# Performance work log

Measured on AMD Instinct MI355X. Metric: run time of the kernel, lower is better.

Reference implementation:

```python
import jax, jax.numpy as jnp
import numpy as np

B, NP, NS, CIN, COUT, CMID = 16, 1024, 32, 64, 128, 32

def _bn(x, g, b, m, v, eps=1e-5):
    # inference-mode BatchNorm over channel axis 1
    sh = (1, -1) + (1,) * (x.ndim - 2)
    return (x - m.reshape(sh)) * (g.reshape(sh) * jax.lax.rsqrt(v.reshape(sh) + eps)) + b.reshape(sh)

def setup_inputs() -> dict:
    key = jax.random.key(0)
    ks = jax.random.split(key, 10)
    f = jax.random.normal
    return {
        "new_xyz": f(ks[0], (B, 3, NP), jnp.float32),
        "grouped_xyz": f(ks[1], (B, NP, NS, 3), jnp.float32),
        "grouped_feature": f(ks[2], (B, CIN, NS, NP), jnp.float32),
        "wh_w": f(ks[3], (CMID, 3), jnp.float32) * 0.1,
        "wh_b": f(ks[4], (CMID,), jnp.float32) * 0.1,
        "wh_g": jnp.ones((CMID,), jnp.float32), "wh_beta": jnp.zeros((CMID,), jnp.float32),
        "wh_m": jnp.zeros((CMID,), jnp.float32), "wh_v": jnp.ones((CMID,), jnp.float32),
        "n1_w": f(ks[5], (16, 1), jnp.float32) * 0.1,
        "n1_b": f(ks[6], (16,), jnp.float32) * 0.1,
        "n1_g": jnp.ones((16,), jnp.float32), "n1_beta": jnp.zeros((16,), jnp.float32),
        "n1_m": jnp.zeros((16,), jnp.float32), "n1_v": jnp.ones((16,), jnp.float32),
        "n2_w": f(ks[7], (1, 16), jnp.float32) * 0.1,
        "n2_b": f(ks[8], (1,), jnp.float32) * 0.1,
        "n2_g": jnp.ones((1,), jnp.float32), "n2_beta": jnp.zeros((1,), jnp.float32),
        "n2_m": jnp.zeros((1,), jnp.float32), "n2_v": jnp.ones((1,), jnp.float32),
        "out_w": f(ks[9], (COUT, CIN, CMID), jnp.float32) * 0.05,
        "out_b": jnp.zeros((COUT,), jnp.float32),
        "out_g": jnp.ones((COUT,), jnp.float32), "out_beta": jnp.zeros((COUT,), jnp.float32),
        "out_m": jnp.zeros((COUT,), jnp.float32), "out_v": jnp.ones((COUT,), jnp.float32),
    }

def reference(new_xyz, grouped_xyz, grouped_feature,
              wh_w, wh_b, wh_g, wh_beta, wh_m, wh_v,
              n1_w, n1_b, n1_g, n1_beta, n1_m, n1_v,
              n2_w, n2_b, n2_g, n2_beta, n2_m, n2_v,
              out_w, out_b, out_g, out_beta, out_m, out_v):
    # kernel_density_estimation_ball mutates in place: after i=0 the reference
    # point is zero, so ONLY sample 0 is actually zeroed. Replicate exactly.
    gx = grouped_xyz.at[:, :, 0, :].set(0.0)          # [B,NP,NS,3]
    density = jnp.sum(gx, axis=-1, keepdims=True)      # [B,NP,NS,1]
    density = jnp.where(density < 1e-10, 1e-10, density)
    inv = 1.0 / density
    ds = inv / jnp.max(inv, axis=2, keepdims=True)     # [B,NP,NS,1]
    # weight net on the mutated grouped_xyz
    gx_p = jnp.transpose(gx, (0, 3, 1, 2))             # [B,3,NP,NS]
    w = jax.nn.relu(_bn(jnp.einsum('bcps,oc->bops', gx_p, wh_w) + wh_b.reshape(1, -1, 1, 1),
                        wh_g, wh_beta, wh_m, wh_v))    # [B,CMID,NP,NS]
    # nonlinear density transform
    dsp = jnp.transpose(ds, (0, 3, 1, 2))              # [B,1,NP,NS]
    d1 = jax.nn.relu(_bn(jnp.einsum('bcps,oc->bops', dsp, n1_w) + n1_b.reshape(1, -1, 1, 1),
                         n1_g, n1_beta, n1_m, n1_v))   # [B,16,NP,NS]
    d2 = jax.nn.sigmoid(_bn(jnp.einsum('bcps,oc->bops', d1, n2_w) + n2_b.reshape(1, -1, 1, 1),
                            n2_g, n2_beta, n2_m, n2_v))  # [B,1,NP,NS]
    # density-scaled features, then batched matmul with positional weights
    gf = jnp.transpose(grouped_feature, (0, 1, 3, 2)) * d2      # [B,CIN,NP,NS]
    mm = jnp.einsum('bcps,bmps->bcpm', gf, w)                   # [B,CIN,NP,CMID]
    # out_conv: Conv2d(CIN->COUT, kernel (1,CMID)) collapses last dim
    out = jnp.einsum('bcpk,ock->bop', mm, out_w) + out_b.reshape(1, -1, 1)  # [B,COUT,NP]
    out = _bn(out, out_g, out_beta, out_m, out_v)
    return (jnp.transpose(new_xyz, (0, 2, 1)), out)
```

## Files before the change

### kernel.cpp

```cpp
#include <hip/hip_runtime.h>
#include <hip/hip_bf16.h>


#define NPP 1024

typedef __attribute__((ext_vector_type(8))) short short8;
typedef __attribute__((ext_vector_type(4))) float f32x4;

__device__ __forceinline__ unsigned short f2bf(float x) {
  union { float f; unsigned u; } v; v.f = x;
  unsigned r = v.u + 0x7FFFu + ((v.u >> 16) & 1u);
  return (unsigned short)(r >> 16);
}

__device__ __forceinline__ unsigned long long pack4bf(f32x4 v) {
  return (unsigned long long)f2bf(v[0])
       | ((unsigned long long)f2bf(v[1]) << 16)
       | ((unsigned long long)f2bf(v[2]) << 32)
       | ((unsigned long long)f2bf(v[3]) << 48);
}

__global__ __launch_bounds__(256) void k_prep(
    const float* __restrict__ out_w, const float* __restrict__ new_xyz,
    unsigned short* __restrict__ owc, float* __restrict__ out0)
{
  int bid = blockIdx.x, t = threadIdx.x;
  if (bid < 128) {
    int gid = bid * 256 + t;
    int lane = gid & 63, ci = gid >> 6;
    int hi = ci & 1, tt = (ci >> 1) & 15, cblk = (ci >> 5) & 3, w = ci >> 7;
    int sg = lane >> 4, l15 = lane & 15;
    int o = w*32 + hi*16 + l15;
    int k = tt*2 + (sg >> 1);
    int cbase = cblk*16 + (sg & 1)*8;
    short8 vv;
    #pragma unroll
    for (int j = 0; j < 8; ++j)
      vv[j] = (short)f2bf(out_w[(o*64 + cbase + j)*32 + k]);
    *(short8*)&owc[(size_t)gid * 8] = vv;
  } else {
    int idx = (bid - 128) * 256 + t;
    int b = idx / 3072, r = idx - b*3072, p = r / 3, d = r - p*3;
    out0[idx] = new_xyz[(b*3 + d)*NPP + p];
  }
}

struct Smem3 {
  union {
    struct {
      float gxd[64*32*4];
      unsigned short wd[16*32*32];
    } ph0;
    unsigned short fs[32768];
  } u;
  char mm[64*1024];
  float cst[192];
};

__global__ __launch_bounds__(512, 1) void k_main(
    const float* __restrict__ F, const float* __restrict__ GX,
    const float* __restrict__ whw, const float* __restrict__ whb,
    const float* __restrict__ whg, const float* __restrict__ whbeta,
    const float* __restrict__ whm, const float* __restrict__ whv,
    const float* __restrict__ n1w, const float* __restrict__ n1b,
    const float* __restrict__ n1g, const float* __restrict__ n1beta,
    const float* __restrict__ n1m, const float* __restrict__ n1v,
    const float* __restrict__ n2w, const float* __restrict__ n2b,
    const float* __restrict__ n2g, const float* __restrict__ n2beta,
    const float* __restrict__ n2m, const float* __restrict__ n2v,
    const unsigned short* __restrict__ OWc,
    const float* __restrict__ ob, const float* __restrict__ og,
    const float* __restrict__ obeta, const float* __restrict__ om,
    const float* __restrict__ ov,
    float* __restrict__ out1)
{
  __shared__ Smem3 sm;
  int xcd = blockIdx.x & 7, idx = blockIdx.x >> 3;
  int b = xcd*2 + (idx >> 4), pt64 = idx & 15;
  int p0 = pt64 * 64;
  int t = threadIdx.x, w = t >> 6, lane = t & 63;
  int l15 = lane & 15, sg = lane >> 4;

  int so = w & 3, ch = w >> 2;
  int q4 = lane & 3, c3 = (lane >> 2) & 7, jh = (lane >> 5) & 1;
  int c_l = ch*8 + c3, s0 = so*8 + jh*4;
  const float* fsrc0 = &F[((size_t)((b*64 + c_l)*32) + s0)*NPP + p0 + q4*4];

  float4 fv[4][4];
  #pragma unroll
  for (int jj = 0; jj < 4; ++jj)
    #pragma unroll
    for (int qg = 0; qg < 4; ++qg)
      fv[jj][qg] = *(const float4*)&fsrc0[(size_t)jj*NPP + qg*16];

  int pp8 = t >> 3, si8 = t & 7;
  const float* g = &GX[(size_t)(b*NPP + p0 + pp8)*96 + si8*12];
  float4 f0 = *(const float4*)g;
  float4 f1 = *(const float4*)(g + 4);
  float4 f2 = *(const float4*)(g + 8);

  if (t < 32) {
    float sc = whg[t] * rsqrtf(whv[t] + 1e-5f);
    sm.cst[t]    = whw[t*3+0] * sc;
    sm.cst[32+t] = whw[t*3+1] * sc;
    sm.cst[64+t] = whw[t*3+2] * sc;
    sm.cst[96+t] = (whb[t] - whm[t]) * sc + whbeta[t];
  } else if (t < 48) {
    int i = t - 32;
    float sc = n1g[i] * rsqrtf(n1v[i] + 1e-5f);
    sm.cst[128+i] = n1w[i] * sc;
    sm.cst[144+i] = (n1b[i] - n1m[i]) * sc + n1beta[i];
  } else if (t < 64) {
    int i = t - 48;
    float sc = n2g[0] * rsqrtf(n2v[0] + 1e-5f);
    sm.cst[160+i] = n2w[i] * sc;
    if (i == 0) sm.cst[176] = (n2b[0] - n2m[0]) * sc + n2beta[0];
  }
  __syncthreads();

  {
    float xs[4], ys[4], zs[4], inv[4];
    xs[0]=f0.x; ys[0]=f0.y; zs[0]=f0.z;
    xs[1]=f0.w; ys[1]=f1.x; zs[1]=f1.y;
    xs[2]=f1.z; ys[2]=f1.w; zs[2]=f2.x;
    xs[3]=f2.y; ys[3]=f2.z; zs[3]=f2.w;
    if (si8 == 0) { xs[0]=0.f; ys[0]=0.f; zs[0]=0.f; }
    float mx = 0.f;
    #pragma unroll
    for (int u = 0; u < 4; ++u) {
      float den = xs[u] + ys[u] + zs[u];
      if (den < 1e-10f) den = 1e-10f;
      inv[u] = 1.0f / den;
      mx = fmaxf(mx, inv[u]);
    }
    #pragma unroll
    for (int m = 1; m < 8; m <<= 1) mx = fmaxf(mx, __shfl_xor(mx, m, 8));
    #pragma unroll
    for (int u = 0; u < 4; ++u) {
      float ds = inv[u] / mx;
      float acc = sm.cst[176];
      #pragma unroll
      for (int i = 0; i < 16; ++i) {
        float d1 = fmaxf(ds * sm.cst[128+i] + sm.cst[144+i], 0.f);
        acc += d1 * sm.cst[160+i];
      }
      float d2 = 1.0f / (1.0f + expf(-acc));
      float4 st = {xs[u], ys[u], zs[u], d2};
      *(float4*)&sm.u.ph0.gxd[(size_t)(pp8*32 + si8*4 + u)*4] = st;
    }
  }
  __syncthreads();

  const f32x4 z4 = {0,0,0,0};
  int phKh = (lane >> 4) & 1;
  int phPp = w*2 + (lane >> 5);
  int phSi = lane & 15;
  int ppA = w*2, ppB = w*2 + 1;
  int c0 = l15*32 + sg*8;

  short8 bfrA[4][2], bfrB[4][2];
  #pragma unroll
  for (int pg = 0; pg < 4; ++pg) {
    const float4 ga = *(const float4*)&sm.u.ph0.gxd[(size_t)((pg*16 + phPp)*32 + phSi*2)*4];
    const float4 gb = *(const float4*)&sm.u.ph0.gxd[(size_t)((pg*16 + phPp)*32 + phSi*2 + 1)*4];
    #pragma unroll
    for (int ki = 0; ki < 16; ++ki) {
      int k = phKh*16 + ki;
      float a0 = sm.cst[k], a1 = sm.cst[32+k], a2 = sm.cst[64+k], bc = sm.cst[96+k];
      float w0 = fmaxf(ga.x*a0 + ga.y*a1 + ga.z*a2 + bc, 0.f) * ga.w;
      float w1 = fmaxf(gb.x*a0 + gb.y*a1 + gb.z*a2 + bc, 0.f) * gb.w;
      unsigned r = (unsigned)f2bf(w0) | ((unsigned)f2bf(w1) << 16);
      *(unsigned*)&sm.u.ph0.wd[(phPp*32 + k)*32 + phSi*2] = r;
    }
    #pragma unroll
    for (int kh = 0; kh < 2; ++kh) {
      bfrA[pg][kh] = *(const short8*)&sm.u.ph0.wd[(ppA*32 + kh*16 + l15)*32 + sg*8];
      bfrB[pg][kh] = *(const short8*)&sm.u.ph0.wd[(ppB*32 + kh*16 + l15)*32 + sg*8];
    }
  }
  __syncthreads();

  int w4 = w & 3, gp0 = (w >> 2) * 2;
  f32x4 acc00 = {0,0,0,0}, acc10 = {0,0,0,0}, acc01 = {0,0,0,0}, acc11 = {0,0,0,0};
  int rowG0 = gp0*16 + l15, rowG1 = (gp0+1)*16 + l15;
  unsigned sw0 = (rowG0 & 15) << 4, sw1 = (rowG1 & 15) << 4;
  const char* bbase0 = sm.mm + rowG0*1024;
  const char* bbase1 = sm.mm + rowG1*1024;
  int fsbase = so*128 + c_l*8 + jh*4;

  #pragma unroll
  for (int cblk = 0; cblk < 4; ++cblk) {
    #pragma unroll
    for (int qg = 0; qg < 4; ++qg)
      #pragma unroll
      for (int pi = 0; pi < 4; ++pi) {
        int p = qg*16 + q4*4 + pi;
        unsigned sw = (unsigned)(p & 15) << 3;
        #pragma unroll
        for (int jp = 0; jp < 2; ++jp) {
          unsigned u = (unsigned)f2bf(((const float*)&fv[jp*2][qg])[pi])
                     | ((unsigned)f2bf(((const float*)&fv[jp*2+1][qg])[pi]) << 16);
          unsigned fidx = (unsigned)(p*512 + fsbase + jp*2) ^ sw;
          *(unsigned*)&sm.u.fs[fidx] = u;
        }
      }
    __syncthreads();

    short8 afA[4], afB[4];
    unsigned swA = (unsigned)(ppA & 15) << 3, swB = (unsigned)(ppB & 15) << 3;
    #pragma unroll
    for (int pg = 0; pg < 4; ++pg) {
      unsigned iA = (unsigned)((pg*16 + ppA)*512 + sg*128 + l15*8) ^ swA;
      unsigned iB = (unsigned)((pg*16 + ppB)*512 + sg*128 + l15*8) ^ swB;
      afA[pg] = *(const short8*)&sm.u.fs[iA];
      afB[pg] = *(const short8*)&sm.u.fs[iB];
    }
    if (cblk < 3) {
      const float* fsrc = fsrc0 + (size_t)(cblk + 1) * 16 * 32 * NPP;
      #pragma unroll
      for (int jj = 0; jj < 4; ++jj)
        #pragma unroll
        for (int qg = 0; qg < 4; ++qg)
          fv[jj][qg] = *(const float4*)&fsrc[(size_t)jj*NPP + qg*16];
    }
    #pragma unroll
    for (int pg = 0; pg < 4; ++pg) {
      f32x4 mA0 = __builtin_amdgcn_mfma_f32_16x16x32_bf16(afA[pg], bfrA[pg][0], z4, 0,0,0);
      f32x4 mA1 = __builtin_amdgcn_mfma_f32_16x16x32_bf16(afA[pg], bfrA[pg][1], z4, 0,0,0);
      f32x4 mB0 = __builtin_amdgcn_mfma_f32_16x16x32_bf16(afB[pg], bfrB[pg][0], z4, 0,0,0);
      f32x4 mB1 = __builtin_amdgcn_mfma_f32_16x16x32_bf16(afB[pg], bfrB[pg][1], z4, 0,0,0);
      int rowA = pg*16 + ppA, rowB = pg*16 + ppB;
      unsigned swa = (rowA & 15) << 4, swb = (rowB & 15) << 4;
      char* bA = sm.mm + rowA*1024;
      char* bB = sm.mm + rowB*1024;
      *(unsigned long long*)(bA + ((c0      ) ^ swa)) = pack4bf(mA0);
      *(unsigned long long*)(bA + ((c0 + 512) ^ swa)) = pack4bf(mA1);
      *(unsigned long long*)(bB + ((c0      ) ^ swb)) = pack4bf(mB0);
      *(unsigned long long*)(bB + ((c0 + 512) ^ swb)) = pack4bf(mB1);
    }
    __syncthreads();
    {
      const unsigned short* ac = &OWc[(size_t)((w4*4 + cblk)*16)*1024 + lane*8];
      #pragma unroll 8
      for (int tt = 0; tt < 16; ++tt) {
        short8 a0 = *(const short8*)&ac[tt*1024];
        short8 a1 = *(const short8*)&ac[tt*1024 + 512];
        int col = sg*16 + tt*64;
        short8 b0 = *(const short8*)(bbase0 + (col ^ sw0));
        short8 b1 = *(const short8*)(bbase1 + (col ^ sw1));
        acc00 = __builtin_amdgcn_mfma_f32_16x16x32_bf16(a0, b0, acc00, 0,0,0);
        acc10 = __builtin_amdgcn_mfma_f32_16x16x32_bf16(a1, b0, acc10, 0,0,0);
        acc01 = __builtin_amdgcn_mfma_f32_16x16x32_bf16(a0, b1, acc01, 0,0,0);
        acc11 = __builtin_amdgcn_mfma_f32_16x16x32_bf16(a1, b1, acc11, 0,0,0);
      }
    }
    __syncthreads();
  }

  #pragma unroll
  for (int hi = 0; hi < 2; ++hi)
    #pragma unroll
    for (int gg = 0; gg < 2; ++gg) {
      f32x4 a = hi ? (gg ? acc11 : acc10) : (gg ? acc01 : acc00);
      #pragma unroll
      for (int r = 0; r < 4; ++r) {
        int o = w4*32 + hi*16 + sg*4 + r;
        float sc = og[o] * rsqrtf(ov[o] + 1e-5f);
        float dd = (ob[o] - om[o]) * sc + obeta[o];
        out1[(size_t)(b*128 + o)*NPP + p0 + (gp0+gg)*16 + l15] = a[r] * sc + dd;
      }
    }
}

extern "C" void kernel_launch(void* const* d_in, const int* in_sizes, int n_in,
                              void* d_out, int out_size, void* d_ws, size_t ws_size,
                              hipStream_t stream) {
  (void)in_sizes; (void)n_in; (void)out_size; (void)ws_size;
  const float* new_xyz = (const float*)d_in[0];
  const float* gxyz    = (const float*)d_in[1];
  const float* gfeat   = (const float*)d_in[2];
  const float* whw     = (const float*)d_in[3];
  const float* whb     = (const float*)d_in[4];
  const float* whg     = (const float*)d_in[5];
  const float* whbeta  = (const float*)d_in[6];
  const float* whm     = (const float*)d_in[7];
  const float* whv     = (const float*)d_in[8];
  const float* n1w     = (const float*)d_in[9];
  const float* n1b     = (const float*)d_in[10];
  const float* n1g     = (const float*)d_in[11];
  const float* n1beta  = (const float*)d_in[12];
  const float* n1m     = (const float*)d_in[13];
  const float* n1v     = (const float*)d_in[14];
  const float* n2w     = (const float*)d_in[15];
  const float* n2b     = (const float*)d_in[16];
  const float* n2g     = (const float*)d_in[17];
  const float* n2beta  = (const float*)d_in[18];
  const float* n2m     = (const float*)d_in[19];
  const float* n2v     = (const float*)d_in[20];
  const float* out_w   = (const float*)d_in[21];
  const float* out_b   = (const float*)d_in[22];
  const float* out_g   = (const float*)d_in[23];
  const float* out_bt  = (const float*)d_in[24];
  const float* out_m   = (const float*)d_in[25];
  const float* out_v   = (const float*)d_in[26];

  unsigned short* owc = (unsigned short*)d_ws;
  float* out0 = (float*)d_out;
  float* out1 = out0 + 16*1024*3;

  hipLaunchKernelGGL(k_prep, dim3(320), dim3(256), 0, stream, out_w, new_xyz, owc, out0);
  hipLaunchKernelGGL(k_main, dim3(256), dim3(512), 0, stream,
      gfeat, gxyz, whw, whb, whg, whbeta, whm, whv,
      n1w, n1b, n1g, n1beta, n1m, n1v,
      n2w, n2b, n2g, n2beta, n2m, n2v,
      owc, out_b, out_g, out_bt, out_m, out_v, out1);
}
```

Baseline: 70.97 us.

## Halve per-block point tile to 32 and shrink LDS for multi-block occupancy

Each block now handles 32 points instead of 64, which doubles the grid to 512 blocks. The LDS layout is reorganised into two unions: one overlaps the gxd and fs buffers, the other overlaps wd and mm. This cuts shared memory per block roughly in half, and launch bounds now ask for 4 blocks per CU. The aim is to fill all CUs with more resident waves and hide the latency of the global feature loads. The cost is that each out_w fragment loaded from global is reused over half as many points, so weight traffic per point doubles, and only half the threads do the density prep.

```diff
diff --git a/kernel.cpp b/kernel.cpp
--- a/kernel.cpp
+++ b/kernel.cpp
@@ -45,19 +45,19 @@
   }
 }
 
-struct Smem3 {
+struct Smem4 {
   union {
-    struct {
-      float gxd[64*32*4];
-      unsigned short wd[16*32*32];
-    } ph0;
-    unsigned short fs[32768];
-  } u;
-  char mm[64*1024];
+    float gxd[32*32*4];
+    unsigned short fs[16384];
+  } a;
+  union {
+    unsigned short wd[16*32*32];
+    char mm[32*1024];
+  } bu;
   float cst[192];
 };
 
-__global__ __launch_bounds__(512, 1) void k_main(
+__global__ __launch_bounds__(512, 4) void k_main(
     const float* __restrict__ F, const float* __restrict__ GX,
     const float* __restrict__ whw, const float* __restrict__ whb,
     const float* __restrict__ whg, const float* __restrict__ whbeta,
@@ -74,10 +74,10 @@
     const float* __restrict__ ov,
     float* __restrict__ out1)
 {
-  __shared__ Smem3 sm;
+  __shared__ Smem4 sm;
   int xcd = blockIdx.x & 7, idx = blockIdx.x >> 3;
-  int b = xcd*2 + (idx >> 4), pt64 = idx & 15;
-  int p0 = pt64 * 64;
+  int b = xcd*2 + (idx >> 5), pt32 = idx & 31;
+  int p0 = pt32 * 32;
   int t = threadIdx.x, w = t >> 6, lane = t & 63;
   int l15 = lane & 15, sg = lane >> 4;
 
@@ -86,18 +86,12 @@
   int c_l = ch*8 + c3, s0 = so*8 + jh*4;
   const float* fsrc0 = &F[((size_t)((b*64 + c_l)*32) + s0)*NPP + p0 + q4*4];
 
-  float4 fv[4][4];
+  float4 fv[4][2];
   #pragma unroll
   for (int jj = 0; jj < 4; ++jj)
     #pragma unroll
-    for (int qg = 0; qg < 4; ++qg)
+    for (int qg = 0; qg < 2; ++qg)
       fv[jj][qg] = *(const float4*)&fsrc0[(size_t)jj*NPP + qg*16];
-
-  int pp8 = t >> 3, si8 = t & 7;
-  const float* g = &GX[(size_t)(b*NPP + p0 + pp8)*96 + si8*12];
-  float4 f0 = *(const float4*)g;
-  float4 f1 = *(const float4*)(g + 4);
-  float4 f2 = *(const float4*)(g + 8);
 
   if (t < 32) {
     float sc = whg[t] * rsqrtf(whv[t] + 1e-5f);
@@ -118,7 +112,12 @@
   }
   __syncthreads();
 
-  {
+  if (t < 256) {
+    int pp8 = t >> 3, si8 = t & 7;
+    const float* g = &GX[(size_t)(b*NPP + p0 + pp8)*96 + si8*12];
+    float4 f0 = *(const float4*)g;
+    float4 f1 = *(const float4*)(g + 4);
+    float4 f2 = *(const float4*)(g + 8);
     float xs[4], ys[4], zs[4], inv[4];
     xs[0]=f0.x; ys[0]=f0.y; zs[0]=f0.z;
     xs[1]=f0.w; ys[1]=f1.x; zs[1]=f1.y;
@@ -146,7 +145,7 @@
       }
       float d2 = 1.0f / (1.0f + expf(-acc));
       float4 st = {xs[u], ys[u], zs[u], d2};
-      *(float4*)&sm.u.ph0.gxd[(size_t)(pp8*32 + si8*4 + u)*4] = st;
+      *(float4*)&sm.a.gxd[(size_t)(pp8*32 + si8*4 + u)*4] = st;
     }
   }
   __syncthreads();
@@ -158,11 +157,11 @@
   int ppA = w*2, ppB = w*2 + 1;
   int c0 = l15*32 + sg*8;
 
-  short8 bfrA[4][2], bfrB[4][2];
+  short8 bfrA[2][2], bfrB[2][2];
   #pragma unroll
-  for (int pg = 0; pg < 4; ++pg) {
-    const float4 ga = *(const float4*)&sm.u.ph0.gxd[(size_t)((pg*16 + phPp)*32 + phSi*2)*4];
-    const float4 gb = *(const float4*)&sm.u.ph0.gxd[(size_t)((pg*16 + phPp)*32 + phSi*2 + 1)*4];
+  for (int pg = 0; pg < 2; ++pg) {
+    const float4 ga = *(const float4*)&sm.a.gxd[(size_t)((pg*16 + phPp)*32 + phSi*2)*4];
+    const float4 gb = *(const float4*)&sm.a.gxd[(size_t)((pg*16 + phPp)*32 + phSi*2 + 1)*4];
     #pragma unroll
     for (int ki = 0; ki < 16; ++ki) {
       int k = phKh*16 + ki;
@@ -170,28 +169,27 @@
       float w0 = fmaxf(ga.x*a0 + ga.y*a1 + ga.z*a2 + bc, 0.f) * ga.w;
       float w1 = fmaxf(gb.x*a0 + gb.y*a1 + gb.z*a2 + bc, 0.f) * gb.w;
       unsigned r = (unsigned)f2bf(w0) | ((unsigned)f2bf(w1) << 16);
-      *(unsigned*)&sm.u.ph0.wd[(phPp*32 + k)*32 + phSi*2] = r;
+      *(unsigned*)&sm.bu.wd[(phPp*32 + k)*32 + phSi*2] = r;
     }
     #pragma unroll
     for (int kh = 0; kh < 2; ++kh) {
-      bfrA[pg][kh] = *(const short8*)&sm.u.ph0.wd[(ppA*32 + kh*16 + l15)*32 + sg*8];
-      bfrB[pg][kh] = *(const short8*)&sm.u.ph0.wd[(ppB*32 + kh*16 + l15)*32 + sg*8];
+      bfrA[pg][kh] = *(const short8*)&sm.bu.wd[(ppA*32 + kh*16 + l15)*32 + sg*8];
+      bfrB[pg][kh] = *(const short8*)&sm.bu.wd[(ppB*32 + kh*16 + l15)*32 + sg*8];
     }
   }
   __syncthreads();
 
-  int w4 = w & 3, gp0 = (w >> 2) * 2;
-  f32x4 acc00 = {0,0,0,0}, acc10 = {0,0,0,0}, acc01 = {0,0,0,0}, acc11 = {0,0,0,0};
-  int rowG0 = gp0*16 + l15, rowG1 = (gp0+1)*16 + l15;
-  unsigned sw0 = (rowG0 & 15) << 4, sw1 = (rowG1 & 15) << 4;
-  const char* bbase0 = sm.mm + rowG0*1024;
-  const char* bbase1 = sm.mm + rowG1*1024;
+  int w4 = w & 3, gp = w >> 2;
+  f32x4 acc0 = {0,0,0,0}, acc1 = {0,0,0,0};
+  int rowG = gp*16 + l15;
+  unsigned swG = (unsigned)(rowG & 15) << 4;
+  const char* bbase = sm.bu.mm + rowG*1024;
   int fsbase = so*128 + c_l*8 + jh*4;
 
   #pragma unroll
   for (int cblk = 0; cblk < 4; ++cblk) {
     #pragma unroll
-    for (int qg = 0; qg < 4; ++qg)
+    for (int qg = 0; qg < 2; ++qg)
       #pragma unroll
       for (int pi = 0; pi < 4; ++pi) {
         int p = qg*16 + q4*4 + pi;
@@ -201,38 +199,38 @@
           unsigned u = (unsigned)f2bf(((const float*)&fv[jp*2][qg])[pi])
                      | ((unsigned)f2bf(((const float*)&fv[jp*2+1][qg])[pi]) << 16);
           unsigned fidx = (unsigned)(p*512 + fsbase + jp*2) ^ sw;
-          *(unsigned*)&sm.u.fs[fidx] = u;
+          *(unsigned*)&sm.a.fs[fidx] = u;
         }
       }
     __syncthreads();
 
-    short8 afA[4], afB[4];
+    short8 afA[2], afB[2];
     unsigned swA = (unsigned)(ppA & 15) << 3, swB = (unsigned)(ppB & 15) << 3;
     #pragma unroll
-    for (int pg = 0; pg < 4; ++pg) {
+    for (int pg = 0; pg < 2; ++pg) {
       unsigned iA = (unsigned)((pg*16 + ppA)*512 + sg*128 + l15*8) ^ swA;
       unsigned iB = (unsigned)((pg*16 + ppB)*512 + sg*128 + l15*8) ^ swB;
-      afA[pg] = *(const short8*)&sm.u.fs[iA];
-      afB[pg] = *(const short8*)&sm.u.fs[iB];
+      afA[pg] = *(const short8*)&sm.a.fs[iA];
+      afB[pg] = *(const short8*)&sm.a.fs[iB];
     }
     if (cblk < 3) {
       const float* fsrc = fsrc0 + (size_t)(cblk + 1) * 16 * 32 * NPP;
       #pragma unroll
       for (int jj = 0; jj < 4; ++jj)
         #pragma unroll
-        for (int qg = 0; qg < 4; ++qg)
+        for (int qg = 0; qg < 2; ++qg)
           fv[jj][qg] = *(const float4*)&fsrc[(size_t)jj*NPP + qg*16];
     }
     #pragma unroll
-    for (int pg = 0; pg < 4; ++pg) {
+    for (int pg = 0; pg < 2; ++pg) {
       f32x4 mA0 = __builtin_amdgcn_mfma_f32_16x16x32_bf16(afA[pg], bfrA[pg][0], z4, 0,0,0);
       f32x4 mA1 = __builtin_amdgcn_mfma_f32_16x16x32_bf16(afA[pg], bfrA[pg][1], z4, 0,0,0);
       f32x4 mB0 = __builtin_amdgcn_mfma_f32_16x16x32_bf16(afB[pg], bfrB[pg][0], z4, 0,0,0);
       f32x4 mB1 = __builtin_amdgcn_mfma_f32_16x16x32_bf16(afB[pg], bfrB[pg][1], z4, 0,0,0);
       int rowA = pg*16 + ppA, rowB = pg*16 + ppB;
-      unsigned swa = (rowA & 15) << 4, swb = (rowB & 15) << 4;
-      char* bA = sm.mm + rowA*1024;
-      char* bB = sm.mm + rowB*1024;
+      unsigned swa = (unsigned)(rowA & 15) << 4, swb = (unsigned)(rowB & 15) << 4;
+      char* bA = sm.bu.mm + rowA*1024;
+      char* bB = sm.bu.mm + rowB*1024;
       *(unsigned long long*)(bA + ((c0      ) ^ swa)) = pack4bf(mA0);
       *(unsigned long long*)(bA + ((c0 + 512) ^ swa)) = pack4bf(mA1);
       *(unsigned long long*)(bB + ((c0      ) ^ swb)) = pack4bf(mB0);
@@ -246,30 +244,25 @@
         short8 a0 = *(const short8*)&ac[tt*1024];
         short8 a1 = *(const short8*)&ac[tt*1024 + 512];
         int col = sg*16 + tt*64;
-        short8 b0 = *(const short8*)(bbase0 + (col ^ sw0));
-        short8 b1 = *(const short8*)(bbase1 + (col ^ sw1));
-        acc00 = __builtin_amdgcn_mfma_f32_16x16x32_bf16(a0, b0, acc00, 0,0,0);
-        acc10 = __builtin_amdgcn_mfma_f32_16x16x32_bf16(a1, b0, acc10, 0,0,0);
-        acc01 = __builtin_amdgcn_mfma_f32_16x16x32_bf16(a0, b1, acc01, 0,0,0);
-        acc11 = __builtin_amdgcn_mfma_f32_16x16x32_bf16(a1, b1, acc11, 0,0,0);
+        short8 bb = *(const short8*)(bbase + (col ^ swG));
+        acc0 = __builtin_amdgcn_mfma_f32_16x16x32_bf16(a0, bb, acc0, 0,0,0);
+        acc1 = __builtin_amdgcn_mfma_f32_16x16x32_bf16(a1, bb, acc1, 0,0,0);
       }
     }
     __syncthreads();
   }
 
   #pragma unroll
-  for (int hi = 0; hi < 2; ++hi)
-    #pragma unroll
-    for (int gg = 0; gg < 2; ++gg) {
-      f32x4 a = hi ? (gg ? acc11 : acc10) : (gg ? acc01 : acc00);
-      #pragma unroll
-      for (int r = 0; r < 4; ++r) {
-        int o = w4*32 + hi*16 + sg*4 + r;
-        float sc = og[o] * rsqrtf(ov[o] + 1e-5f);
-        float dd = (ob[o] - om[o]) * sc + obeta[o];
-        out1[(size_t)(b*128 + o)*NPP + p0 + (gp0+gg)*16 + l15] = a[r] * sc + dd;
-      }
-    }
+  for (int hi = 0; hi < 2; ++hi) {
+    f32x4 a = hi ? acc1 : acc0;
+    #pragma unroll
+    for (int r = 0; r < 4; ++r) {
+      int o = w4*32 + hi*16 + sg*4 + r;
+      float sc = og[o] * rsqrtf(ov[o] + 1e-5f);
+      float dd = (ob[o] - om[o]) * sc + obeta[o];
+      out1[(size_t)(b*128 + o)*NPP + p0 + gp*16 + l15] = a[r] * sc + dd;
+    }
+  }
 }
 
 extern "C" void kernel_launch(void* const* d_in, const int* in_sizes, int n_in,
@@ -309,7 +302,7 @@
   float* out1 = out0 + 16*1024*3;
 
   hipLaunchKernelGGL(k_prep, dim3(320), dim3(256), 0, stream, out_w, new_xyz, owc, out0);
-  hipLaunchKernelGGL(k_main, dim3(256), dim3(512), 0, stream,
+  hipLaunchKernelGGL(k_main, dim3(512), dim3(512), 0, stream,
       gfeat, gxyz, whw, whb, whg, whbeta, whm, whv,
       n1w, n1b, n1g, n1beta, n1m, n1v,
       n2w, n2b, n2g, n2beta, n2m, n2v,
```

Result: slower. 76.16 us (+7.3%).

## Split fused kernel into two stages with global bf16 intermediate

Applied to the files above, without the earlier changes.

The single fused kernel is split. The first stage computes the density-weighted feature-by-positional-weight matmul and writes the bf16 result to a global workspace. A second kernel with 1024 blocks of 256 threads then loads it into LDS and runs the output-conv MFMA plus BatchNorm. This is meant to remove the serialized second GEMM and the extra barriers inside each 256-block kernel, and to give stage 2 more parallelism. In exchange it adds a global write and read of the intermediate (about 64MB of bf16) and one more kernel launch.

```diff
diff --git a/kernel.cpp b/kernel.cpp
--- a/kernel.cpp
+++ b/kernel.cpp
@@ -45,7 +45,7 @@
   }
 }
 
-struct Smem3 {
+struct SmemS1 {
   union {
     struct {
       float gxd[64*32*4];
@@ -53,11 +53,10 @@
     } ph0;
     unsigned short fs[32768];
   } u;
-  char mm[64*1024];
   float cst[192];
 };
 
-__global__ __launch_bounds__(512, 1) void k_main(
+__global__ __launch_bounds__(512, 1) void k_stage1(
     const float* __restrict__ F, const float* __restrict__ GX,
     const float* __restrict__ whw, const float* __restrict__ whb,
     const float* __restrict__ whg, const float* __restrict__ whbeta,
@@ -68,13 +67,9 @@
     const float* __restrict__ n2w, const float* __restrict__ n2b,
     const float* __restrict__ n2g, const float* __restrict__ n2beta,
     const float* __restrict__ n2m, const float* __restrict__ n2v,
-    const unsigned short* __restrict__ OWc,
-    const float* __restrict__ ob, const float* __restrict__ og,
-    const float* __restrict__ obeta, const float* __restrict__ om,
-    const float* __restrict__ ov,
-    float* __restrict__ out1)
+    unsigned short* __restrict__ mmG)
 {
-  __shared__ Smem3 sm;
+  __shared__ SmemS1 sm;
   int xcd = blockIdx.x & 7, idx = blockIdx.x >> 3;
   int b = xcd*2 + (idx >> 4), pt64 = idx & 15;
   int p0 = pt64 * 64;
@@ -156,7 +151,6 @@
   int phPp = w*2 + (lane >> 5);
   int phSi = lane & 15;
   int ppA = w*2, ppB = w*2 + 1;
-  int c0 = l15*32 + sg*8;
 
   short8 bfrA[4][2], bfrB[4][2];
   #pragma unroll
@@ -180,12 +174,6 @@
   }
   __syncthreads();
 
-  int w4 = w & 3, gp0 = (w >> 2) * 2;
-  f32x4 acc00 = {0,0,0,0}, acc10 = {0,0,0,0}, acc01 = {0,0,0,0}, acc11 = {0,0,0,0};
-  int rowG0 = gp0*16 + l15, rowG1 = (gp0+1)*16 + l15;
-  unsigned sw0 = (rowG0 & 15) << 4, sw1 = (rowG1 & 15) << 4;
-  const char* bbase0 = sm.mm + rowG0*1024;
-  const char* bbase1 = sm.mm + rowG1*1024;
   int fsbase = so*128 + c_l*8 + jh*4;
 
   #pragma unroll
@@ -229,47 +217,74 @@
       f32x4 mA1 = __builtin_amdgcn_mfma_f32_16x16x32_bf16(afA[pg], bfrA[pg][1], z4, 0,0,0);
       f32x4 mB0 = __builtin_amdgcn_mfma_f32_16x16x32_bf16(afB[pg], bfrB[pg][0], z4, 0,0,0);
       f32x4 mB1 = __builtin_amdgcn_mfma_f32_16x16x32_bf16(afB[pg], bfrB[pg][1], z4, 0,0,0);
-      int rowA = pg*16 + ppA, rowB = pg*16 + ppB;
-      unsigned swa = (rowA & 15) << 4, swb = (rowB & 15) << 4;
-      char* bA = sm.mm + rowA*1024;
-      char* bB = sm.mm + rowB*1024;
-      *(unsigned long long*)(bA + ((c0      ) ^ swa)) = pack4bf(mA0);
-      *(unsigned long long*)(bA + ((c0 + 512) ^ swa)) = pack4bf(mA1);
-      *(unsigned long long*)(bB + ((c0      ) ^ swb)) = pack4bf(mB0);
-      *(unsigned long long*)(bB + ((c0 + 512) ^ swb)) = pack4bf(mB1);
+      int pA = p0 + pg*16 + ppA, pB = p0 + pg*16 + ppB;
+      unsigned short* gA = &mmG[(size_t)(b*1024 + pA)*2048 + cblk*512 + l15*16 + sg*4];
+      unsigned short* gB = &mmG[(size_t)(b*1024 + pB)*2048 + cblk*512 + l15*16 + sg*4];
+      *(unsigned long long*)(gA)       = pack4bf(mA0);
+      *(unsigned long long*)(gA + 256) = pack4bf(mA1);
+      *(unsigned long long*)(gB)       = pack4bf(mB0);
+      *(unsigned long long*)(gB + 256) = pack4bf(mB1);
     }
     __syncthreads();
-    {
-      const unsigned short* ac = &OWc[(size_t)((w4*4 + cblk)*16)*1024 + lane*8];
-      #pragma unroll 8
-      for (int tt = 0; tt < 16; ++tt) {
-        short8 a0 = *(const short8*)&ac[tt*1024];
-        short8 a1 = *(const short8*)&ac[tt*1024 + 512];
-        int col = sg*16 + tt*64;
-        short8 b0 = *(const short8*)(bbase0 + (col ^ sw0));
-        short8 b1 = *(const short8*)(bbase1 + (col ^ sw1));
-        acc00 = __builtin_amdgcn_mfma_f32_16x16x32_bf16(a0, b0, acc00, 0,0,0);
-        acc10 = __builtin_amdgcn_mfma_f32_16x16x32_bf16(a1, b0, acc10, 0,0,0);
-        acc01 = __builtin_amdgcn_mfma_f32_16x16x32_bf16(a0, b1, acc01, 0,0,0);
-        acc11 = __builtin_amdgcn_mfma_f32_16x16x32_bf16(a1, b1, acc11, 0,0,0);
-      }
-    }
-    __syncthreads();
-  }
-
-  #pragma unroll
-  for (int hi = 0; hi < 2; ++hi)
-    #pragma unroll
-    for (int gg = 0; gg < 2; ++gg) {
-      f32x4 a = hi ? (gg ? acc11 : acc10) : (gg ? acc01 : acc00);
-      #pragma unroll
-      for (int r = 0; r < 4; ++r) {
-        int o = w4*32 + hi*16 + sg*4 + r;
-        float sc = og[o] * rsqrtf(ov[o] + 1e-5f);
-        float dd = (ob[o] - om[o]) * sc + obeta[o];
-        out1[(size_t)(b*128 + o)*NPP + p0 + (gp0+gg)*16 + l15] = a[r] * sc + dd;
-      }
-    }
+  }
+}
+
+__global__ __launch_bounds__(256, 2) void k_stage2(
+    const unsigned short* __restrict__ OWc,
+    const unsigned short* __restrict__ mmG,
+    const float* __restrict__ ob, const float* __restrict__ og,
+    const float* __restrict__ obeta, const float* __restrict__ om,
+    const float* __restrict__ ov,
+    float* __restrict__ out1)
+{
+  __shared__ unsigned short ms[16*2048];
+  int xcd = blockIdx.x & 7, idx = blockIdx.x >> 3;
+  int b = xcd*2 + (idx >> 6), ptile = idx & 63;
+  int p0 = ptile * 16;
+  int t = threadIdx.x, w = t >> 6, lane = t & 63;
+  int l15 = lane & 15, sg = lane >> 4;
+
+  #pragma unroll
+  for (int i = 0; i < 4; ++i) {
+    int pl = i*4 + w;
+    const unsigned short* src = &mmG[(size_t)(b*1024 + p0 + pl)*2048 + lane*8];
+    #pragma unroll
+    for (int j = 0; j < 4; ++j) {
+      short8 v = *(const short8*)&src[j*512];
+      unsigned off = ((unsigned)(pl*4096 + lane*16 + j*1024)) ^ ((unsigned)(pl & 15) << 4);
+      *(short8*)((char*)ms + off) = v;
+    }
+  }
+  __syncthreads();
+
+  f32x4 acc0 = {0,0,0,0}, acc1 = {0,0,0,0};
+  unsigned swR = (unsigned)(l15 & 15) << 4;
+  const char* brow = (const char*)ms + l15*4096;
+  #pragma unroll
+  for (int cblk = 0; cblk < 4; ++cblk) {
+    const unsigned short* ac = &OWc[(size_t)((w*4 + cblk)*16)*1024 + lane*8];
+    #pragma unroll 8
+    for (int tt = 0; tt < 16; ++tt) {
+      short8 a0 = *(const short8*)&ac[tt*1024];
+      short8 a1 = *(const short8*)&ac[tt*1024 + 512];
+      unsigned col = (unsigned)(cblk*1024 + tt*64 + sg*16) ^ swR;
+      short8 bb = *(const short8*)(brow + col);
+      acc0 = __builtin_amdgcn_mfma_f32_16x16x32_bf16(a0, bb, acc0, 0,0,0);
+      acc1 = __builtin_amdgcn_mfma_f32_16x16x32_bf16(a1, bb, acc1, 0,0,0);
+    }
+  }
+
+  #pragma unroll
+  for (int hi = 0; hi < 2; ++hi) {
+    f32x4 a = hi ? acc1 : acc0;
+    #pragma unroll
+    for (int r = 0; r < 4; ++r) {
+      int o = w*32 + hi*16 + sg*4 + r;
+      float sc = og[o] * rsqrtf(ov[o] + 1e-5f);
+      float dd = (ob[o] - om[o]) * sc + obeta[o];
+      out1[(size_t)(b*128 + o)*NPP + p0 + l15] = a[r] * sc + dd;
+    }
+  }
 }
 
 extern "C" void kernel_launch(void* const* d_in, const int* in_sizes, int n_in,
@@ -305,13 +320,15 @@
   const float* out_v   = (const float*)d_in[26];
 
   unsigned short* owc = (unsigned short*)d_ws;
+  unsigned short* mmG = owc + (1u << 18);
   float* out0 = (float*)d_out;
   float* out1 = out0 + 16*1024*3;
 
-  hipLaunchKernelGGL(k_prep, dim3(320), dim3(256), 0, stream, out_w, new_xyz, owc, out0);
-  hipLaunchKernelGGL(k_main, dim3(256), dim3(512), 0, stream,
+  hipLaunchKernelGGL(k_prep,   dim3(320),  dim3(256), 0, stream, out_w, new_xyz, owc, out0);
+  hipLaunchKernelGGL(k_stage1, dim3(256),  dim3(512), 0, stream,
       gfeat, gxyz, whw, whb, whg, whbeta, whm, whv,
       n1w, n1b, n1g, n1beta, n1m, n1v,
-      n2w, n2b, n2g, n2beta, n2m, n2v,
-      owc, out_b, out_g, out_bt, out_m, out_v, out1);
-}
+      n2w, n2b, n2g, n2beta, n2m, n2v, mmG);
+  hipLaunchKernelGGL(k_stage2, dim3(1024), dim3(256), 0, stream,
+      owc, mmG, out_b, out_g, out_bt, out_m, out_v, out1);
+}
```

Result: slower. 94.77 us (+33.5%).

## Alias mm buffer onto feature staging LDS and drop register prefetch to raise occupancy

Applied to the files above, without the earlier changes.

Removes the separate 64KB mm shared buffer by reusing the feature staging buffer, which needs an extra barrier between reading the A fragments and writing mm. The 64-float4 register prefetch of the next channel block is dropped; features are loaded in two halves right before conversion. Launch bounds change to allow more blocks per CU. This trades the overlap of global loads with compute for lower LDS and register use, so several blocks can hide latency instead.

```diff
diff --git a/kernel.cpp b/kernel.cpp
--- a/kernel.cpp
+++ b/kernel.cpp
@@ -45,19 +45,18 @@
   }
 }
 
-struct Smem3 {
+struct Smem6 {
   union {
     struct {
       float gxd[64*32*4];
       unsigned short wd[16*32*32];
     } ph0;
-    unsigned short fs[32768];
+    unsigned short fsmm[32768];
   } u;
-  char mm[64*1024];
   float cst[192];
 };
 
-__global__ __launch_bounds__(512, 1) void k_main(
+__global__ __launch_bounds__(512, 4) void k_main(
     const float* __restrict__ F, const float* __restrict__ GX,
     const float* __restrict__ whw, const float* __restrict__ whb,
     const float* __restrict__ whg, const float* __restrict__ whbeta,
@@ -74,7 +73,7 @@
     const float* __restrict__ ov,
     float* __restrict__ out1)
 {
-  __shared__ Smem3 sm;
+  __shared__ Smem6 sm;
   int xcd = blockIdx.x & 7, idx = blockIdx.x >> 3;
   int b = xcd*2 + (idx >> 4), pt64 = idx & 15;
   int p0 = pt64 * 64;
@@ -85,13 +84,6 @@
   int q4 = lane & 3, c3 = (lane >> 2) & 7, jh = (lane >> 5) & 1;
   int c_l = ch*8 + c3, s0 = so*8 + jh*4;
   const float* fsrc0 = &F[((size_t)((b*64 + c_l)*32) + s0)*NPP + p0 + q4*4];
-
-  float4 fv[4][4];
-  #pragma unroll
-  for (int jj = 0; jj < 4; ++jj)
-    #pragma unroll
-    for (int qg = 0; qg < 4; ++qg)
-      fv[jj][qg] = *(const float4*)&fsrc0[(size_t)jj*NPP + qg*16];
 
   int pp8 = t >> 3, si8 = t & 7;
   const float* g = &GX[(size_t)(b*NPP + p0 + pp8)*96 + si8*12];
@@ -184,26 +176,36 @@
   f32x4 acc00 = {0,0,0,0}, acc10 = {0,0,0,0}, acc01 = {0,0,0,0}, acc11 = {0,0,0,0};
   int rowG0 = gp0*16 + l15, rowG1 = (gp0+1)*16 + l15;
   unsigned sw0 = (rowG0 & 15) << 4, sw1 = (rowG1 & 15) << 4;
-  const char* bbase0 = sm.mm + rowG0*1024;
-  const char* bbase1 = sm.mm + rowG1*1024;
+  const char* bbase0 = (const char*)sm.u.fsmm + rowG0*1024;
+  const char* bbase1 = (const char*)sm.u.fsmm + rowG1*1024;
   int fsbase = so*128 + c_l*8 + jh*4;
 
   #pragma unroll
   for (int cblk = 0; cblk < 4; ++cblk) {
     #pragma unroll
-    for (int qg = 0; qg < 4; ++qg)
+    for (int half = 0; half < 2; ++half) {
+      float4 fvh[4][2];
+      const float* fsrc = fsrc0 + (size_t)cblk * 16 * 32 * NPP;
       #pragma unroll
-      for (int pi = 0; pi < 4; ++pi) {
-        int p = qg*16 + q4*4 + pi;
-        unsigned sw = (unsigned)(p & 15) << 3;
+      for (int jj = 0; jj < 4; ++jj)
         #pragma unroll
-        for (int jp = 0; jp < 2; ++jp) {
-          unsigned u = (unsigned)f2bf(((const float*)&fv[jp*2][qg])[pi])
-                     | ((unsigned)f2bf(((const float*)&fv[jp*2+1][qg])[pi]) << 16);
-          unsigned fidx = (unsigned)(p*512 + fsbase + jp*2) ^ sw;
-          *(unsigned*)&sm.u.fs[fidx] = u;
+        for (int qh = 0; qh < 2; ++qh)
+          fvh[jj][qh] = *(const float4*)&fsrc[(size_t)jj*NPP + (half*2 + qh)*16];
+      #pragma unroll
+      for (int qh = 0; qh < 2; ++qh)
+        #pragma unroll
+        for (int pi = 0; pi < 4; ++pi) {
+          int p = (half*2 + qh)*16 + q4*4 + pi;
+          unsigned sw = (unsigned)(p & 15) << 3;
+          #pragma unroll
+          for (int jp = 0; jp < 2; ++jp) {
+            unsigned u = (unsigned)f2bf(((const float*)&fvh[jp*2][qh])[pi])
+                       | ((unsigned)f2bf(((const float*)&fvh[jp*2+1][qh])[pi]) << 16);
+            unsigned fidx = (unsigned)(p*512 + fsbase + jp*2) ^ sw;
+            *(unsigned*)&sm.u.fsmm[fidx] = u;
+          }
         }
-      }
+    }
     __syncthreads();
 
     short8 afA[4], afB[4];
@@ -212,17 +214,11 @@
     for (int pg = 0; pg < 4; ++pg) {
       unsigned iA = (unsigned)((pg*16 + ppA)*512 + sg*128 + l15*8) ^ swA;
       unsigned iB = (unsigned)((pg*16 + ppB)*512 + sg*128 + l15*8) ^ swB;
-      afA[pg] = *(const short8*)&sm.u.fs[iA];
-      afB[pg] = *(const short8*)&sm.u.fs[iB];
-    }
-    if (cblk < 3) {
-      const float* fsrc = fsrc0 + (size_t)(cblk + 1) * 16 * 32 * NPP;
-      #pragma unroll
-      for (int jj = 0; jj < 4; ++jj)
-        #pragma unroll
-        for (int qg = 0; qg < 4; ++qg)
-          fv[jj][qg] = *(const float4*)&fsrc[(size_t)jj*NPP + qg*16];
-    }
+      afA[pg] = *(const short8*)&sm.u.fsmm[iA];
+      afB[pg] = *(const short8*)&sm.u.fsmm[iB];
+    }
+    __syncthreads();
+
     #pragma unroll
     for (int pg = 0; pg < 4; ++pg) {
       f32x4 mA0 = __builtin_amdgcn_mfma_f32_16x16x32_bf16(afA[pg], bfrA[pg][0], z4, 0,0,0);
@@ -231,14 +227,15 @@
       f32x4 mB1 = __builtin_amdgcn_mfma_f32_16x16x32_bf16(afB[pg], bfrB[pg][1], z4, 0,0,0);
       int rowA = pg*16 + ppA, rowB = pg*16 + ppB;
       unsigned swa = (rowA & 15) << 4, swb = (rowB & 15) << 4;
-      char* bA = sm.mm + rowA*1024;
-      char* bB = sm.mm + rowB*1024;
+      char* bA = (char*)sm.u.fsmm + rowA*1024;
+      char* bB = (char*)sm.u.fsmm + rowB*1024;
       *(unsigned long long*)(bA + ((c0      ) ^ swa)) = pack4bf(mA0);
       *(unsigned long long*)(bA + ((c0 + 512) ^ swa)) = pack4bf(mA1);
       *(unsigned long long*)(bB + ((c0      ) ^ swb)) = pack4bf(mB0);
       *(unsigned long long*)(bB + ((c0 + 512) ^ swb)) = pack4bf(mB1);
     }
     __syncthreads();
+
     {
       const unsigned short* ac = &OWc[(size_t)((w4*4 + cblk)*16)*1024 + lane*8];
       #pragma unroll 8
```

Result: slower. 111.1 us (+56.6%).
